# Kernel optimization log

Hardware: AMD Instinct MI355X
Metric: run time of the kernel (lower is better)

Reference implementation:

```python
import jax, jax.numpy as jnp
import numpy as np
import math

B, C, H, W = 512, 64, 8, 8
E, NH, MEM = 64, 8, 8          # embed_dim, num_heads, mem_n
HD = E // NH                   # head_dim
THD = H * W * HD               # tot_head_dim = 512
AMB = 5.0                      # attn_mask_b
LN_EPS = 1e-5


def conv2d(x, w, b):
    y = jax.lax.conv_general_dilated(x, w, (1, 1), 'SAME',
                                     dimension_numbers=('NCHW', 'OIHW', 'NCHW'))
    return y + b[None, :, None, None]


def setup_inputs() -> dict:
    key = jax.random.key(0)
    ks = jax.random.split(key, 14)
    r = lambda k, s, sc=1.0: jax.random.normal(k, s, dtype=jnp.float32) * sc
    return {
        'input': r(ks[0], (B, C, H, W)),
        'h_cur': r(ks[1], (B, E, H, W)),
        'c_cur': r(ks[2], (B, E, H, W)),
        'concat_k': r(ks[3], (B, MEM, NH, THD)),
        'concat_v': r(ks[4], (B, MEM, NH, THD)),
        'attn_mask': jax.random.randint(ks[5], (B * NH, 1, MEM), 0, 2).astype(bool),
        'conv_w': r(ks[6], (5 * E, C + E, 3, 3), 0.05),
        'conv_b': jnp.zeros((5 * E,), jnp.float32),
        'proj_w': r(ks[7], (3 * E, C, 3, 3), 0.05),
        'proj_b': jnp.zeros((3 * E,), jnp.float32),
        'out_w': r(ks[8], (E, E, 3, 3), 0.05),
        'out_b': jnp.zeros((E,), jnp.float32),
        'ln_w': jnp.ones((E, H, W), jnp.float32),
        'ln_b': jnp.zeros((E, H, W), jnp.float32),
        'pos_w': r(ks[9], (MEM, H * W * E), 0.02),
        'pos_b': jax.random.uniform(ks[10], (MEM, NH), jnp.float32, -0.1, 0.1),
    }


def _cell(input, h_cur, c_cur, concat_k, concat_v, attn_mask,
          conv_w, conv_b, proj_w, proj_b, out_w, out_b, ln_w, ln_b, pos_w, pos_b):
    # ConvLSTM gates
    combined = jnp.concatenate([input, h_cur], axis=1)          # [B, C+E, H, W]
    cc = conv2d(combined, conv_w, conv_b)                       # [B, 5E, H, W]
    cc_i, cc_f, cc_o, cc_g, cc_a = jnp.split(cc, 5, axis=1)
    i = jax.nn.sigmoid(cc_i)
    f = jax.nn.sigmoid(cc_f)
    o = jax.nn.sigmoid(cc_o)
    g = jnp.tanh(cc_g)
    a = jax.nn.sigmoid(cc_a)
    c_next = f * c_cur + i * g

    # attention over growing memory
    kqv = conv2d(input, proj_w, proj_b)                         # [B, 3E, H, W]
    k, q, v = jnp.split(kqv, 3, axis=1)
    # [B, E, H, W] -> [B*NH, 1, THD] (contiguous split of E into NH heads)
    resh = lambda x: x.reshape(B * NH, 1, THD)
    k, q, v = resh(k), resh(q), resh(v)
    q_scaled = q / math.sqrt(THD)

    # prior memory: [B, MEM, NH, THD] -> [B*NH, MEM-1, THD]
    def mem_resh(m):
        return jnp.transpose(m[:, 1:], (1, 0, 2, 3)).reshape(MEM - 1, B * NH, THD).transpose(1, 0, 2)
    k_full = jnp.concatenate([mem_resh(concat_k), k], axis=1)   # [B*NH, MEM, THD]
    v_full = jnp.concatenate([mem_resh(concat_v), v], axis=1)

    # learned positional key offsets / score biases
    pos_w_e = jnp.broadcast_to(pos_w[:, None, :], (MEM, B, H * W * E)) \
                 .reshape(MEM, B * NH, THD).transpose(1, 0, 2)  # [B*NH, MEM, THD]
    pos_b_e = jnp.broadcast_to(pos_b[:, None, :], (MEM, B, NH)) \
                 .reshape(MEM, B * NH).T                        # [B*NH, MEM]
    k_full = k_full + pos_w_e

    # additive mask: -inf where masked, last slot forced to +attn_mask_b
    mask = jnp.where(attn_mask, -jnp.inf, 0.0).astype(q.dtype)  # [B*NH, 1, MEM]
    mask = mask.at[:, :, -1].set(AMB)

    scores = mask + jnp.einsum('bqd,bkd->bqk', q_scaled, k_full) + pos_b_e[:, None, :]
    w = jax.nn.softmax(scores, axis=-1)                         # [B*NH, 1, MEM]
    attn = jnp.einsum('bqk,bkd->bqd', w, v_full)                # [B*NH, 1, THD]
    attn = attn.reshape(B, E, H, W)

    out = conv2d(attn, out_w, out_b) + input[:, :E]
    # LayerNorm over (E, H, W)
    mu = jnp.mean(out, axis=(1, 2, 3), keepdims=True)
    var = jnp.mean((out - mu) ** 2, axis=(1, 2, 3), keepdims=True)
    out = (out - mu) / jnp.sqrt(var + LN_EPS) * ln_w[None] + ln_b[None]

    c_next = c_next + a * jnp.tanh(out)
    h_next = o * jnp.tanh(c_next)

    ret = lambda m: m.transpose(1, 0, 2).reshape(MEM, B, NH, THD).transpose(1, 0, 2, 3)
    return h_next, c_next, ret(k_full), ret(v_full)


def reference(input, h_cur, c_cur, concat_k, concat_v, attn_mask,
              conv_w, conv_b, proj_w, proj_b, out_w, out_b, ln_w, ln_b, pos_w, pos_b):
    return _cell(input, h_cur, c_cur, concat_k, concat_v, attn_mask,
                 conv_w, conv_b, proj_w, proj_b, out_w, out_b, ln_w, ln_b, pos_w, pos_b)
```

## Files before the change

### kernel.cpp

```cpp
#include <hip/hip_runtime.h>

typedef short short8 __attribute__((ext_vector_type(8)));
typedef __bf16 bf16x8 __attribute__((ext_vector_type(8)));
typedef float f32x4 __attribute__((ext_vector_type(4)));

__device__ __forceinline__ short f2bf(float f) {
  unsigned u = __builtin_bit_cast(unsigned, f);
  u = (u + 0x7FFFu + ((u >> 16) & 1u)) >> 16;
  return (short)u;
}
__device__ __forceinline__ f32x4 mfma16(short8 a, short8 b, f32x4 c) {
  return __builtin_amdgcn_mfma_f32_16x16x32_bf16(
      __builtin_bit_cast(bf16x8, a), __builtin_bit_cast(bf16x8, b), c, 0, 0, 0);
}
__device__ __forceinline__ float sigm(float x) { return 1.0f / (1.0f + __expf(-x)); }
__device__ __forceinline__ float ftanh(float x) {
  return 1.0f - 2.0f / (1.0f + __expf(2.0f * x));
}
__device__ __forceinline__ f32x4 ntld4(const float* p) {
  return __builtin_nontemporal_load((const f32x4*)p);
}
__device__ __forceinline__ void ntst4(float* p, f32x4 v) {
  __builtin_nontemporal_store(v, (f32x4*)p);
}

__global__ void pack_w(const float* __restrict__ w1, const float* __restrict__ w2,
                       const float* __restrict__ w3, short* __restrict__ out) {
  int e = blockIdx.x * 256 + threadIdx.x;
  if (e < 46080) {
    int kb8 = e / 320, n = e % 320;
    short8 v;
#pragma unroll
    for (int j = 0; j < 8; ++j) {
      int k = kb8 * 8 + j;
      int tap = k >> 7, ci = k & 127;
      v[j] = f2bf(w1[(n * 128 + ci) * 9 + tap]);
    }
    *(short8*)&out[e * 8] = v;
    return;
  }
  e -= 46080;
  if (e < 13824) {
    int kb8 = e / 192, n = e % 192;
    short8 v;
#pragma unroll
    for (int j = 0; j < 8; ++j) {
      int k = kb8 * 8 + j;
      int tap = k >> 6, ci = k & 63;
      v[j] = f2bf(w2[(n * 64 + ci) * 9 + tap]);
    }
    *(short8*)&out[(46080 + e) * 8] = v;
    return;
  }
  e -= 13824;
  {
    int kb8 = e / 64, n = e % 64;
    short8 v;
#pragma unroll
    for (int j = 0; j < 8; ++j) {
      int k = kb8 * 8 + j;
      int tap = k >> 6, ci = k & 63;
      v[j] = f2bf(w3[(n * 64 + ci) * 9 + tap]);
    }
    *(short8*)&out[(46080 + 13824 + e) * 8] = v;
  }
}

__launch_bounds__(512, 4)
__global__ void kqv_k(const float* __restrict__ input,
                      const float* __restrict__ proj_b,
                      const float* __restrict__ pos_w,
                      const short* __restrict__ pk2,
                      float* __restrict__ q_out, float* __restrict__ o_k,
                      float* __restrict__ o_v) {
  __shared__ short comb[6400];
  __shared__ float Xk[4160], Xq[4160], Xv[4160];

  const int b = blockIdx.x;
  const int tid = threadIdx.x;
  const int wave = tid >> 6, lane = tid & 63;
  const int col = lane & 15, g4 = lane >> 4;
  const int wc = wave >> 1, wm = wave & 1;
  const int ch = wc * 16 + col;

#pragma unroll
  for (int i = 0; i < 2; ++i) {
    int idx = (tid + 512 * i) * 4;
    int c = idx >> 6, p0 = idx & 63;
    f32x4 vi = *(const f32x4*)&input[b * 4096 + idx];
#pragma unroll
    for (int j = 0; j < 4; ++j) {
      int p = p0 + j;
      int pp = ((p >> 3) + 1) * 10 + (p & 7) + 1;
      comb[pp * 64 + ((c + pp * 8) & 63)] = f2bf(vi[j]);
    }
  }
  for (int i = tid; i < 2304; i += 512) {
    int pr = i >> 6, c = i & 63;
    int pp = (pr < 10) ? pr
             : (pr < 20) ? (80 + pr)
             : (pr < 28) ? ((pr - 19) * 10)
                         : ((pr - 27) * 10 + 9);
    comb[pp * 64 + c] = 0;
  }
  __syncthreads();

  f32x4 acc2[2][3];
#pragma unroll
  for (int m = 0; m < 2; ++m)
#pragma unroll
    for (int g = 0; g < 3; ++g) acc2[m][g] = (f32x4){0.f, 0.f, 0.f, 0.f};

  short8 bb2[3];
#pragma unroll
  for (int g = 0; g < 3; ++g)
    bb2[g] = *(const short8*)&pk2[((g4)*192 + g * 64 + ch) * 8];

  for (int s = 0; s < 18; ++s) {
    short8 bbn[3];
    if (s < 17) {
      int kb8 = (s + 1) * 4 + g4;
#pragma unroll
      for (int g = 0; g < 3; ++g)
        bbn[g] = *(const short8*)&pk2[(kb8 * 192 + g * 64 + ch) * 8];
    }
    int tap = s >> 1, cib = s & 1;
    int kh = tap / 3, kw = tap % 3;
    short8 a[2];
#pragma unroll
    for (int m = 0; m < 2; ++m) {
      int p = (wm * 2 + m) * 16 + col;
      int pp = ((p >> 3) + kh) * 10 + (p & 7) + kw;
      int slot = (cib * 32 + g4 * 8 + pp * 8) & 63;
      a[m] = *(const short8*)&comb[pp * 64 + slot];
    }
#pragma unroll
    for (int m = 0; m < 2; ++m)
#pragma unroll
      for (int g = 0; g < 3; ++g) acc2[m][g] = mfma16(a[m], bb2[g], acc2[m][g]);
    if (s < 17) {
#pragma unroll
      for (int g = 0; g < 3; ++g) bb2[g] = bbn[g];
    }
  }
  {
    float pb0 = proj_b[ch], pb1 = proj_b[64 + ch], pb2 = proj_b[128 + ch];
    const float rsq = 0.044194173824159216f;
#pragma unroll
    for (int m = 0; m < 2; ++m)
#pragma unroll
      for (int r = 0; r < 4; ++r) {
        int p = (wm * 2 + m) * 16 + g4 * 4 + r;
        Xk[ch * 65 + p] = acc2[m][0][r] + pb0 + pos_w[7 * 4096 + ch * 64 + p];
        Xq[ch * 65 + p] = (acc2[m][1][r] + pb1) * rsq;
        Xv[ch * 65 + p] = acc2[m][2][r] + pb2;
      }
  }
  __syncthreads();

  const size_t base7 = (size_t)(b * 64 + 56) * 512;
#pragma unroll
  for (int i = 0; i < 2; ++i) {
    int idx = (tid + 512 * i) * 4;
    int c = idx >> 6, p0 = idx & 63;
    f32x4 kq, qq, vq;
#pragma unroll
    for (int j = 0; j < 4; ++j) {
      kq[j] = Xk[c * 65 + p0 + j];
      qq[j] = Xq[c * 65 + p0 + j];
      vq[j] = Xv[c * 65 + p0 + j];
    }
    *(f32x4*)&o_k[base7 + idx] = kq;
    *(f32x4*)&q_out[(size_t)b * 4096 + idx] = qq;
    *(f32x4*)&o_v[base7 + idx] = vq;
  }
}

__launch_bounds__(64, 4)
__global__ void attn_k(const float* __restrict__ ck, const float* __restrict__ cv,
                       const int* __restrict__ amask,
                       const float* __restrict__ pos_w,
                       const float* __restrict__ pos_b,
                       const float* __restrict__ q_in,
                       float* __restrict__ o_k, float* __restrict__ o_v,
                       float* __restrict__ attn_out) {
  const int b = blockIdx.x >> 3;
  const int hd = blockIdx.x & 7;
  const int lane = threadIdx.x;
  const int d0 = lane * 4, d1 = (lane + 64) * 4;

  const float* qp = q_in + (size_t)b * 4096 + hd * 512;
  f32x4 q0 = *(const f32x4*)&qp[d0];
  f32x4 q1 = *(const f32x4*)&qp[d1];

  float sc[8];
#pragma unroll
  for (int m = 0; m < 7; ++m) {
    const float* kp = ck + ((size_t)((b * 8 + m + 1) * 8 + hd)) * 512;
    const float* pw = pos_w + m * 4096 + hd * 512;
    f32x4 k0 = ntld4(kp + d0) + *(const f32x4*)&pw[d0];
    f32x4 k1 = ntld4(kp + d1) + *(const f32x4*)&pw[d1];
    float* dst = o_k + ((size_t)((b * 8 + m) * 8 + hd)) * 512;
    ntst4(dst + d0, k0);
    ntst4(dst + d1, k1);
    float part = 0.f;
#pragma unroll
    for (int j = 0; j < 4; ++j) {
      part = fmaf(q0[j], k0[j], part);
      part = fmaf(q1[j], k1[j], part);
    }
#pragma unroll
    for (int off = 32; off >= 1; off >>= 1) part += __shfl_xor(part, off);
    float msk = amask[(b * 8 + hd) * 8 + m] ? -__builtin_inff() : 0.0f;
    sc[m] = part + pos_b[m * 8 + hd] + msk;
  }
  {
    const float* kp = o_k + ((size_t)((b * 8 + 7) * 8 + hd)) * 512;
    f32x4 k0 = *(const f32x4*)&kp[d0];
    f32x4 k1 = *(const f32x4*)&kp[d1];
    float part = 0.f;
#pragma unroll
    for (int j = 0; j < 4; ++j) {
      part = fmaf(q0[j], k0[j], part);
      part = fmaf(q1[j], k1[j], part);
    }
#pragma unroll
    for (int off = 32; off >= 1; off >>= 1) part += __shfl_xor(part, off);
    sc[7] = part + pos_b[7 * 8 + hd] + 5.0f;
  }

  float mx = sc[0];
#pragma unroll
  for (int m = 1; m < 8; ++m) mx = fmaxf(mx, sc[m]);
  float w[8], s = 0.f;
#pragma unroll
  for (int m = 0; m < 8; ++m) {
    w[m] = __expf(sc[m] - mx);
    s += w[m];
  }
  float inv = 1.0f / s;
#pragma unroll
  for (int m = 0; m < 8; ++m) w[m] *= inv;

  f32x4 a0 = (f32x4){0.f, 0.f, 0.f, 0.f};
  f32x4 a1 = (f32x4){0.f, 0.f, 0.f, 0.f};
#pragma unroll
  for (int m = 0; m < 7; ++m) {
    const float* vp = cv + ((size_t)((b * 8 + m + 1) * 8 + hd)) * 512;
    f32x4 v0 = ntld4(vp + d0);
    f32x4 v1 = ntld4(vp + d1);
    float* dst = o_v + ((size_t)((b * 8 + m) * 8 + hd)) * 512;
    ntst4(dst + d0, v0);
    ntst4(dst + d1, v1);
    a0 += v0 * w[m];
    a1 += v1 * w[m];
  }
  {
    const float* vp = o_v + ((size_t)((b * 8 + 7) * 8 + hd)) * 512;
    a0 += *(const f32x4*)&vp[d0] * w[7];
    a1 += *(const f32x4*)&vp[d1] * w[7];
  }
  float* ap = attn_out + (size_t)b * 4096 + hd * 512;
  *(f32x4*)&ap[d0] = a0;
  *(f32x4*)&ap[d1] = a1;
}

__launch_bounds__(512, 4)
__global__ void cell2_k(
    const float* __restrict__ input, const float* __restrict__ h_cur,
    const float* __restrict__ c_cur, const float* __restrict__ attn_in,
    const float* __restrict__ conv_b, const float* __restrict__ out_b,
    const float* __restrict__ ln_w, const float* __restrict__ ln_b,
    const short* __restrict__ pk1, const short* __restrict__ pk3,
    float* __restrict__ o_h, float* __restrict__ o_c) {
  __shared__ short comb[12800];
  __shared__ float Xb[4160];
  __shared__ float Qb[4160];
  __shared__ float Vb[4160];
  __shared__ float red[16];

  const int b = blockIdx.x;
  const int tid = threadIdx.x;
  const int wave = tid >> 6, lane = tid & 63;
  const int col = lane & 15, g4 = lane >> 4;
  const int wc = wave >> 1, wm = wave & 1;
  const int ch = wc * 16 + col;

#pragma unroll
  for (int i = 0; i < 2; ++i) {
    int idx = (tid + 512 * i) * 4;
    int c = idx >> 6, p0 = idx & 63;
    f32x4 vi = *(const f32x4*)&input[b * 4096 + idx];
    f32x4 vh = *(const f32x4*)&h_cur[b * 4096 + idx];
    f32x4 vc = *(const f32x4*)&c_cur[b * 4096 + idx];
#pragma unroll
    for (int j = 0; j < 4; ++j) {
      int p = p0 + j;
      int pp = ((p >> 3) + 1) * 10 + (p & 7) + 1;
      comb[pp * 128 + ((c + pp * 8) & 127)] = f2bf(vi[j]);
      comb[pp * 128 + ((c + 64 + pp * 8) & 127)] = f2bf(vh[j]);
      Xb[c * 65 + p] = vc[j];
    }
  }
  for (int i = tid; i < 4608; i += 512) {
    int pr = i >> 7, c = i & 127;
    int pp = (pr < 10) ? pr
             : (pr < 20) ? (80 + pr)
             : (pr < 28) ? ((pr - 19) * 10)
                         : ((pr - 27) * 10 + 9);
    comb[pp * 128 + c] = 0;
  }
  __syncthreads();

  f32x4 acc1[2][5];
#pragma unroll
  for (int m = 0; m < 2; ++m)
#pragma unroll
    for (int g = 0; g < 5; ++g) acc1[m][g] = (f32x4){0.f, 0.f, 0.f, 0.f};

  short8 bb1[5];
#pragma unroll
  for (int g = 0; g < 5; ++g)
    bb1[g] = *(const short8*)&pk1[((g4)*320 + g * 64 + ch) * 8];

  for (int s = 0; s < 36; ++s) {
    short8 bbn[5];
    if (s < 35) {
      int kb8 = (s + 1) * 4 + g4;
#pragma unroll
      for (int g = 0; g < 5; ++g)
        bbn[g] = *(const short8*)&pk1[(kb8 * 320 + g * 64 + ch) * 8];
    }
    int tap = s >> 2, cib = s & 3;
    int kh = tap / 3, kw = tap % 3;
    short8 a[2];
#pragma unroll
    for (int m = 0; m < 2; ++m) {
      int p = (wm * 2 + m) * 16 + col;
      int pp = ((p >> 3) + kh) * 10 + (p & 7) + kw;
      int slot = (cib * 32 + g4 * 8 + pp * 8) & 127;
      a[m] = *(const short8*)&comb[pp * 128 + slot];
    }
#pragma unroll
    for (int m = 0; m < 2; ++m)
#pragma unroll
      for (int g = 0; g < 5; ++g) acc1[m][g] = mfma16(a[m], bb1[g], acc1[m][g]);
    if (s < 35) {
#pragma unroll
      for (int g = 0; g < 5; ++g) bb1[g] = bbn[g];
    }
  }

  float ct_r[8], o_r[8], a_r[8];
  {
    float bi0 = conv_b[ch], bi1 = conv_b[64 + ch], bi2 = conv_b[128 + ch];
    float bi3 = conv_b[192 + ch], bi4 = conv_b[256 + ch];
#pragma unroll
    for (int m = 0; m < 2; ++m)
#pragma unroll
      for (int r = 0; r < 4; ++r) {
        int p = (wm * 2 + m) * 16 + g4 * 4 + r;
        float iv = sigm(acc1[m][0][r] + bi0);
        float fv = sigm(acc1[m][1][r] + bi1);
        float ov = sigm(acc1[m][2][r] + bi2);
        float gv = ftanh(acc1[m][3][r] + bi3);
        float av = sigm(acc1[m][4][r] + bi4);
        ct_r[m * 4 + r] = fv * Xb[ch * 65 + p] + iv * gv;
        o_r[m * 4 + r] = ov;
        a_r[m * 4 + r] = av;
      }
  }
  __syncthreads();

  {
    f32x4 av[2], iv[2];
#pragma unroll
    for (int i = 0; i < 2; ++i) {
      int idx = (tid + 512 * i) * 4;
      av[i] = *(const f32x4*)&attn_in[b * 4096 + idx];
      iv[i] = *(const f32x4*)&input[b * 4096 + idx];
    }
#pragma unroll
    for (int i = 0; i < 2; ++i) {
      int idx = (tid + 512 * i) * 4;
      int c = idx >> 6, p0 = idx & 63;
#pragma unroll
      for (int j = 0; j < 4; ++j) {
        int p = p0 + j;
        int pp = ((p >> 3) + 1) * 10 + (p & 7) + 1;
        comb[pp * 128 + ((c + pp * 8) & 127)] = f2bf(av[i][j]);
        Xb[c * 65 + p] = iv[i][j];
      }
    }
  }
  __syncthreads();

  f32x4 acc3[2];
  acc3[0] = (f32x4){0.f, 0.f, 0.f, 0.f};
  acc3[1] = (f32x4){0.f, 0.f, 0.f, 0.f};
  short8 bb3 = *(const short8*)&pk3[((g4)*64 + ch) * 8];
  for (int s = 0; s < 18; ++s) {
    short8 bbn;
    if (s < 17) {
      int kb8 = (s + 1) * 4 + g4;
      bbn = *(const short8*)&pk3[(kb8 * 64 + ch) * 8];
    }
    int tap = s >> 1, cib = s & 1;
    int kh = tap / 3, kw = tap % 3;
    short8 a[2];
#pragma unroll
    for (int m = 0; m < 2; ++m) {
      int p = (wm * 2 + m) * 16 + col;
      int pp = ((p >> 3) + kh) * 10 + (p & 7) + kw;
      int slot = (cib * 32 + g4 * 8 + pp * 8) & 127;
      a[m] = *(const short8*)&comb[pp * 128 + slot];
    }
#pragma unroll
    for (int m = 0; m < 2; ++m) acc3[m] = mfma16(a[m], bb3, acc3[m]);
    if (s < 17) bb3 = bbn;
  }

  float ov_[8], s1 = 0.f, s2 = 0.f;
  {
    float ob = out_b[ch];
#pragma unroll
    for (int m = 0; m < 2; ++m)
#pragma unroll
      for (int r = 0; r < 4; ++r) {
        int p = (wm * 2 + m) * 16 + g4 * 4 + r;
        float v = acc3[m][r] + ob + Xb[ch * 65 + p];
        ov_[m * 4 + r] = v;
        s1 += v;
        s2 += v * v;
      }
  }
#pragma unroll
  for (int off = 32; off >= 1; off >>= 1) {
    s1 += __shfl_xor(s1, off);
    s2 += __shfl_xor(s2, off);
  }
  if (lane == 0) { red[wave] = s1; red[8 + wave] = s2; }
  __syncthreads();
  float ts1 = 0.f, ts2 = 0.f;
#pragma unroll
  for (int w = 0; w < 8; ++w) { ts1 += red[w]; ts2 += red[8 + w]; }
  float mu = ts1 * (1.0f / 4096.0f);
  float var = ts2 * (1.0f / 4096.0f) - mu * mu;
  float rstd = rsqrtf(var + 1e-5f);

#pragma unroll
  for (int m = 0; m < 2; ++m)
#pragma unroll
    for (int r = 0; r < 4; ++r) {
      int p = (wm * 2 + m) * 16 + g4 * 4 + r;
      float oln = (ov_[m * 4 + r] - mu) * rstd * ln_w[ch * 64 + p] + ln_b[ch * 64 + p];
      float cn = ct_r[m * 4 + r] + a_r[m * 4 + r] * ftanh(oln);
      float hv = o_r[m * 4 + r] * ftanh(cn);
      Qb[ch * 65 + p] = hv;
      Vb[ch * 65 + p] = cn;
    }
  __syncthreads();
#pragma unroll
  for (int i = 0; i < 2; ++i) {
    int idx = (tid + 512 * i) * 4;
    int c = idx >> 6, p0 = idx & 63;
    f32x4 hv, cvv;
#pragma unroll
    for (int j = 0; j < 4; ++j) {
      hv[j] = Qb[c * 65 + p0 + j];
      cvv[j] = Vb[c * 65 + p0 + j];
    }
    *(f32x4*)&o_h[b * 4096 + idx] = hv;
    *(f32x4*)&o_c[b * 4096 + idx] = cvv;
  }
}

extern "C" void kernel_launch(void* const* d_in, const int* in_sizes, int n_in,
                              void* d_out, int out_size, void* d_ws, size_t ws_size,
                              hipStream_t stream) {
  (void)in_sizes; (void)n_in; (void)out_size; (void)ws_size;
  const float* input  = (const float*)d_in[0];
  const float* h_cur  = (const float*)d_in[1];
  const float* c_cur  = (const float*)d_in[2];
  const float* ck     = (const float*)d_in[3];
  const float* cv     = (const float*)d_in[4];
  const int*   amask  = (const int*)d_in[5];
  const float* conv_w = (const float*)d_in[6];
  const float* conv_b = (const float*)d_in[7];
  const float* proj_w = (const float*)d_in[8];
  const float* proj_b = (const float*)d_in[9];
  const float* out_w  = (const float*)d_in[10];
  const float* out_b  = (const float*)d_in[11];
  const float* ln_w   = (const float*)d_in[12];
  const float* ln_b   = (const float*)d_in[13];
  const float* pos_w  = (const float*)d_in[14];
  const float* pos_b  = (const float*)d_in[15];

  short* pk = (short*)d_ws;
  float* o_h = (float*)d_out;
  float* o_c = o_h + 2097152;
  float* o_k = o_h + 4194304;
  float* o_v = o_h + 20971520;

  pack_w<<<252, 256, 0, stream>>>(conv_w, proj_w, out_w, pk);
  kqv_k<<<512, 512, 0, stream>>>(input, proj_b, pos_w, pk + 368640,
                                 o_h, o_k, o_v);
  attn_k<<<4096, 64, 0, stream>>>(ck, cv, amask, pos_w, pos_b, o_h,
                                  o_k, o_v, o_c);
  cell2_k<<<512, 512, 0, stream>>>(input, h_cur, c_cur, o_c,
                                   conv_b, out_b, ln_w, ln_b,
                                   pk, pk + 479232, o_h, o_c);
}
```

Before: 113.7 us.

## Restructure into mid kernel fusing kqv+attention alongside gate conv, plus back kernel

Replaces the kqv/attn/cell2 chain with two kernels. The first runs 1024 blocks: half compute the k/q/v projection conv and then the full attention per batch item in the same block, and the other half compute the ConvLSTM gate conv, writing c_t and packed bf16 o/a gates to workspace. The second kernel does the output conv, LayerNorm and the final cell update. This removes one launch and the q round-trip through global memory, and lets the gate conv run concurrently with attention. In exchange it adds workspace traffic for the attention output, c_t and gates, stores gates and attention output in bf16 (lower precision), and falls back to the old path when the workspace is too small.

```diff
diff --git a/kernel.cpp b/kernel.cpp
--- a/kernel.cpp
+++ b/kernel.cpp
@@ -3,6 +3,8 @@
 typedef short short8 __attribute__((ext_vector_type(8)));
 typedef __bf16 bf16x8 __attribute__((ext_vector_type(8)));
 typedef float f32x4 __attribute__((ext_vector_type(4)));
+typedef short s16x4 __attribute__((ext_vector_type(4)));
+typedef unsigned u32x4 __attribute__((ext_vector_type(4)));
 
 __device__ __forceinline__ short f2bf(float f) {
   unsigned u = __builtin_bit_cast(unsigned, f);
@@ -63,6 +65,490 @@
       v[j] = f2bf(w3[(n * 64 + ci) * 9 + tap]);
     }
     *(short8*)&out[(46080 + 13824 + e) * 8] = v;
+  }
+}
+
+
+__launch_bounds__(512, 4)
+__global__ void mid_k(const float* __restrict__ input, const float* __restrict__ h_cur,
+                      const float* __restrict__ c_cur, const float* __restrict__ ck,
+                      const float* __restrict__ cv, const int* __restrict__ amask,
+                      const float* __restrict__ conv_b, const float* __restrict__ proj_b,
+                      const float* __restrict__ pos_w, const float* __restrict__ pos_b,
+                      const short* __restrict__ pk1, const short* __restrict__ pk2,
+                      float* __restrict__ o_k, float* __restrict__ o_v,
+                      short* __restrict__ ws_attn, float* __restrict__ ws_ct,
+                      unsigned* __restrict__ ws_oa) {
+  __shared__ short comb[12800];
+  __shared__ float Xb[4160];
+  __shared__ float sc_lds[8];
+  float* combf = (float*)comb;
+  unsigned* Xbu = (unsigned*)Xb;
+
+  const int tid = threadIdx.x;
+  const int wave = tid >> 6, lane = tid & 63;
+  const int col = lane & 15, g4 = lane >> 4;
+  const int wc = wave >> 1, wm = wave & 1;
+  const int ch = wc * 16 + col;
+
+  if (blockIdx.x < 512) {
+    const int b = blockIdx.x;
+    if (tid < 8) sc_lds[tid] = 0.f;
+
+#pragma unroll
+    for (int i = 0; i < 2; ++i) {
+      int idx = (tid + 512 * i) * 4;
+      int c = idx >> 6, p0 = idx & 63;
+      f32x4 vi = *(const f32x4*)&input[b * 4096 + idx];
+#pragma unroll
+      for (int j = 0; j < 4; ++j) {
+        int p = p0 + j;
+        int pp = ((p >> 3) + 1) * 10 + (p & 7) + 1;
+        comb[pp * 64 + ((c + pp * 8) & 63)] = f2bf(vi[j]);
+      }
+    }
+    for (int i = tid; i < 2304; i += 512) {
+      int pr = i >> 6, c = i & 63;
+      int pp = (pr < 10) ? pr
+               : (pr < 20) ? (80 + pr)
+               : (pr < 28) ? ((pr - 19) * 10)
+                           : ((pr - 27) * 10 + 9);
+      comb[pp * 64 + c] = 0;
+    }
+    __syncthreads();
+
+    f32x4 acc2[2][3];
+#pragma unroll
+    for (int m = 0; m < 2; ++m)
+#pragma unroll
+      for (int g = 0; g < 3; ++g) acc2[m][g] = (f32x4){0.f, 0.f, 0.f, 0.f};
+    short8 bb2[3];
+#pragma unroll
+    for (int g = 0; g < 3; ++g)
+      bb2[g] = *(const short8*)&pk2[((g4)*192 + g * 64 + ch) * 8];
+    for (int s = 0; s < 18; ++s) {
+      short8 bbn[3];
+      if (s < 17) {
+        int kb8 = (s + 1) * 4 + g4;
+#pragma unroll
+        for (int g = 0; g < 3; ++g)
+          bbn[g] = *(const short8*)&pk2[(kb8 * 192 + g * 64 + ch) * 8];
+      }
+      int tap = s >> 1, cib = s & 1;
+      int kh = tap / 3, kw = tap % 3;
+      short8 a[2];
+#pragma unroll
+      for (int m = 0; m < 2; ++m) {
+        int p = (wm * 2 + m) * 16 + col;
+        int pp = ((p >> 3) + kh) * 10 + (p & 7) + kw;
+        int slot = (cib * 32 + g4 * 8 + pp * 8) & 63;
+        a[m] = *(const short8*)&comb[pp * 64 + slot];
+      }
+#pragma unroll
+      for (int m = 0; m < 2; ++m)
+#pragma unroll
+        for (int g = 0; g < 3; ++g) acc2[m][g] = mfma16(a[m], bb2[g], acc2[m][g]);
+      if (s < 17) {
+#pragma unroll
+        for (int g = 0; g < 3; ++g) bb2[g] = bbn[g];
+      }
+    }
+
+    float kreg[8], qreg[8], vreg[8], part7 = 0.f;
+    {
+      float pb0 = proj_b[ch], pb1 = proj_b[64 + ch], pb2 = proj_b[128 + ch];
+      const float rsq = 0.044194173824159216f;
+#pragma unroll
+      for (int m = 0; m < 2; ++m)
+#pragma unroll
+        for (int r = 0; r < 4; ++r) {
+          int p = (wm * 2 + m) * 16 + g4 * 4 + r;
+          float kf = acc2[m][0][r] + pb0 + pos_w[7 * 4096 + ch * 64 + p];
+          float qf = (acc2[m][1][r] + pb1) * rsq;
+          float vf = acc2[m][2][r] + pb2;
+          kreg[m * 4 + r] = kf;
+          qreg[m * 4 + r] = qf;
+          vreg[m * 4 + r] = vf;
+          part7 = fmaf(qf, kf, part7);
+        }
+    }
+    atomicAdd(&sc_lds[ch >> 3], part7);
+    __syncthreads();
+
+#pragma unroll
+    for (int m = 0; m < 2; ++m)
+#pragma unroll
+      for (int r = 0; r < 4; ++r) {
+        int p = (wm * 2 + m) * 16 + g4 * 4 + r;
+        combf[ch * 65 + p] = kreg[m * 4 + r];
+        Xb[ch * 65 + p] = qreg[m * 4 + r];
+      }
+    __syncthreads();
+
+    const size_t base7 = (size_t)(b * 64 + 56) * 512;
+#pragma unroll
+    for (int i = 0; i < 2; ++i) {
+      int idx = (tid + 512 * i) * 4;
+      int c = idx >> 6, p0 = idx & 63;
+      f32x4 kq;
+#pragma unroll
+      for (int j = 0; j < 4; ++j) kq[j] = combf[c * 65 + p0 + j];
+      ntst4(&o_k[base7 + idx], kq);
+    }
+    const int hd = wave;
+    const int d0 = lane * 4, d1 = (lane + 64) * 4;
+    const int cs0 = d0 >> 6, po0 = d0 & 63, cs1 = d1 >> 6, po1 = d1 & 63;
+    f32x4 q0, q1;
+#pragma unroll
+    for (int j = 0; j < 4; ++j) {
+      q0[j] = Xb[(hd * 8 + cs0) * 65 + po0 + j];
+      q1[j] = Xb[(hd * 8 + cs1) * 65 + po1 + j];
+    }
+    float sc7 = sc_lds[hd] + pos_b[7 * 8 + hd] + 5.0f;
+    __syncthreads();
+
+#pragma unroll
+    for (int m = 0; m < 2; ++m)
+#pragma unroll
+      for (int r = 0; r < 4; ++r) {
+        int p = (wm * 2 + m) * 16 + g4 * 4 + r;
+        combf[ch * 65 + p] = vreg[m * 4 + r];
+      }
+    __syncthreads();
+#pragma unroll
+    for (int i = 0; i < 2; ++i) {
+      int idx = (tid + 512 * i) * 4;
+      int c = idx >> 6, p0 = idx & 63;
+      f32x4 vq;
+#pragma unroll
+      for (int j = 0; j < 4; ++j) vq[j] = combf[c * 65 + p0 + j];
+      ntst4(&o_v[base7 + idx], vq);
+    }
+    f32x4 v70, v71;
+#pragma unroll
+    for (int j = 0; j < 4; ++j) {
+      v70[j] = combf[(hd * 8 + cs0) * 65 + po0 + j];
+      v71[j] = combf[(hd * 8 + cs1) * 65 + po1 + j];
+    }
+
+    float scv[8];
+    scv[7] = sc7;
+#pragma unroll
+    for (int m = 0; m < 7; ++m) {
+      const float* kp = ck + ((size_t)((b * 8 + m + 1) * 8 + hd)) * 512;
+      const float* pw = pos_w + m * 4096 + hd * 512;
+      f32x4 k0 = ntld4(kp + d0) + *(const f32x4*)&pw[d0];
+      f32x4 k1 = ntld4(kp + d1) + *(const f32x4*)&pw[d1];
+      float* dst = o_k + ((size_t)((b * 8 + m) * 8 + hd)) * 512;
+      ntst4(dst + d0, k0);
+      ntst4(dst + d1, k1);
+      float part = 0.f;
+#pragma unroll
+      for (int j = 0; j < 4; ++j) {
+        part = fmaf(q0[j], k0[j], part);
+        part = fmaf(q1[j], k1[j], part);
+      }
+#pragma unroll
+      for (int off = 32; off >= 1; off >>= 1) part += __shfl_xor(part, off);
+      float msk = amask[(b * 8 + hd) * 8 + m] ? -__builtin_inff() : 0.0f;
+      scv[m] = part + pos_b[m * 8 + hd] + msk;
+    }
+    float mx = scv[0];
+#pragma unroll
+    for (int m = 1; m < 8; ++m) mx = fmaxf(mx, scv[m]);
+    float w[8], s = 0.f;
+#pragma unroll
+    for (int m = 0; m < 8; ++m) {
+      w[m] = __expf(scv[m] - mx);
+      s += w[m];
+    }
+    float inv = 1.0f / s;
+#pragma unroll
+    for (int m = 0; m < 8; ++m) w[m] *= inv;
+
+    f32x4 a0 = (f32x4){0.f, 0.f, 0.f, 0.f};
+    f32x4 a1 = (f32x4){0.f, 0.f, 0.f, 0.f};
+#pragma unroll
+    for (int m = 0; m < 7; ++m) {
+      const float* vp = cv + ((size_t)((b * 8 + m + 1) * 8 + hd)) * 512;
+      f32x4 v0 = ntld4(vp + d0);
+      f32x4 v1 = ntld4(vp + d1);
+      float* dst = o_v + ((size_t)((b * 8 + m) * 8 + hd)) * 512;
+      ntst4(dst + d0, v0);
+      ntst4(dst + d1, v1);
+      a0 += v0 * w[m];
+      a1 += v1 * w[m];
+    }
+    a0 += v70 * w[7];
+    a1 += v71 * w[7];
+
+    s16x4 s0, s1;
+#pragma unroll
+    for (int j = 0; j < 4; ++j) {
+      s0[j] = f2bf(a0[j]);
+      s1[j] = f2bf(a1[j]);
+    }
+    *(s16x4*)&ws_attn[(size_t)b * 4096 + hd * 512 + d0] = s0;
+    *(s16x4*)&ws_attn[(size_t)b * 4096 + hd * 512 + d1] = s1;
+  } else {
+    const int b = blockIdx.x - 512;
+#pragma unroll
+    for (int i = 0; i < 2; ++i) {
+      int idx = (tid + 512 * i) * 4;
+      int c = idx >> 6, p0 = idx & 63;
+      f32x4 vi = *(const f32x4*)&input[b * 4096 + idx];
+      f32x4 vh = *(const f32x4*)&h_cur[b * 4096 + idx];
+      f32x4 vc = *(const f32x4*)&c_cur[b * 4096 + idx];
+#pragma unroll
+      for (int j = 0; j < 4; ++j) {
+        int p = p0 + j;
+        int pp = ((p >> 3) + 1) * 10 + (p & 7) + 1;
+        comb[pp * 128 + ((c + pp * 8) & 127)] = f2bf(vi[j]);
+        comb[pp * 128 + ((c + 64 + pp * 8) & 127)] = f2bf(vh[j]);
+        Xb[c * 65 + p] = vc[j];
+      }
+    }
+    for (int i = tid; i < 4608; i += 512) {
+      int pr = i >> 7, c = i & 127;
+      int pp = (pr < 10) ? pr
+               : (pr < 20) ? (80 + pr)
+               : (pr < 28) ? ((pr - 19) * 10)
+                           : ((pr - 27) * 10 + 9);
+      comb[pp * 128 + c] = 0;
+    }
+    __syncthreads();
+
+    f32x4 acc1[2][5];
+#pragma unroll
+    for (int m = 0; m < 2; ++m)
+#pragma unroll
+      for (int g = 0; g < 5; ++g) acc1[m][g] = (f32x4){0.f, 0.f, 0.f, 0.f};
+    short8 bb1[5];
+#pragma unroll
+    for (int g = 0; g < 5; ++g)
+      bb1[g] = *(const short8*)&pk1[((g4)*320 + g * 64 + ch) * 8];
+    for (int s = 0; s < 36; ++s) {
+      short8 bbn[5];
+      if (s < 35) {
+        int kb8 = (s + 1) * 4 + g4;
+#pragma unroll
+        for (int g = 0; g < 5; ++g)
+          bbn[g] = *(const short8*)&pk1[(kb8 * 320 + g * 64 + ch) * 8];
+      }
+      int tap = s >> 2, cib = s & 3;
+      int kh = tap / 3, kw = tap % 3;
+      short8 a[2];
+#pragma unroll
+      for (int m = 0; m < 2; ++m) {
+        int p = (wm * 2 + m) * 16 + col;
+        int pp = ((p >> 3) + kh) * 10 + (p & 7) + kw;
+        int slot = (cib * 32 + g4 * 8 + pp * 8) & 127;
+        a[m] = *(const short8*)&comb[pp * 128 + slot];
+      }
+#pragma unroll
+      for (int m = 0; m < 2; ++m)
+#pragma unroll
+        for (int g = 0; g < 5; ++g) acc1[m][g] = mfma16(a[m], bb1[g], acc1[m][g]);
+      if (s < 35) {
+#pragma unroll
+        for (int g = 0; g < 5; ++g) bb1[g] = bbn[g];
+      }
+    }
+
+    float ctv[8];
+    unsigned oav[8];
+    {
+      float bi0 = conv_b[ch], bi1 = conv_b[64 + ch], bi2 = conv_b[128 + ch];
+      float bi3 = conv_b[192 + ch], bi4 = conv_b[256 + ch];
+#pragma unroll
+      for (int m = 0; m < 2; ++m)
+#pragma unroll
+        for (int r = 0; r < 4; ++r) {
+          int p = (wm * 2 + m) * 16 + g4 * 4 + r;
+          float iv = sigm(acc1[m][0][r] + bi0);
+          float fv = sigm(acc1[m][1][r] + bi1);
+          float ov = sigm(acc1[m][2][r] + bi2);
+          float gv = ftanh(acc1[m][3][r] + bi3);
+          float av = sigm(acc1[m][4][r] + bi4);
+          ctv[m * 4 + r] = fv * Xb[ch * 65 + p] + iv * gv;
+          oav[m * 4 + r] = ((unsigned)(unsigned short)f2bf(av) << 16) |
+                           (unsigned)(unsigned short)f2bf(ov);
+        }
+    }
+    __syncthreads();
+#pragma unroll
+    for (int m = 0; m < 2; ++m)
+#pragma unroll
+      for (int r = 0; r < 4; ++r) {
+        int p = (wm * 2 + m) * 16 + g4 * 4 + r;
+        combf[ch * 65 + p] = ctv[m * 4 + r];
+        Xbu[ch * 65 + p] = oav[m * 4 + r];
+      }
+    __syncthreads();
+#pragma unroll
+    for (int i = 0; i < 2; ++i) {
+      int idx = (tid + 512 * i) * 4;
+      int c = idx >> 6, p0 = idx & 63;
+      f32x4 cq;
+      u32x4 oq;
+#pragma unroll
+      for (int j = 0; j < 4; ++j) {
+        cq[j] = combf[c * 65 + p0 + j];
+        oq[j] = Xbu[c * 65 + p0 + j];
+      }
+      *(f32x4*)&ws_ct[(size_t)b * 4096 + idx] = cq;
+      *(u32x4*)&ws_oa[(size_t)b * 4096 + idx] = oq;
+    }
+  }
+}
+
+__launch_bounds__(512, 4)
+__global__ void back_k(const float* __restrict__ input,
+                       const short* __restrict__ ws_attn,
+                       const float* __restrict__ ws_ct,
+                       const unsigned* __restrict__ ws_oa,
+                       const float* __restrict__ out_b,
+                       const float* __restrict__ ln_w, const float* __restrict__ ln_b,
+                       const short* __restrict__ pk3,
+                       float* __restrict__ o_h, float* __restrict__ o_c) {
+  __shared__ short comb[8320];
+  __shared__ float Xb[4160];
+  __shared__ float red[16];
+  float* combf = (float*)comb;
+  unsigned* Xbu = (unsigned*)Xb;
+
+  const int b = blockIdx.x;
+  const int tid = threadIdx.x;
+  const int wave = tid >> 6, lane = tid & 63;
+  const int col = lane & 15, g4 = lane >> 4;
+  const int wc = wave >> 1, wm = wave & 1;
+  const int ch = wc * 16 + col;
+
+  f32x4 ctr[2];
+  u32x4 oar[2];
+#pragma unroll
+  for (int i = 0; i < 2; ++i) {
+    int idx = (tid + 512 * i) * 4;
+    ctr[i] = *(const f32x4*)&ws_ct[(size_t)b * 4096 + idx];
+    oar[i] = *(const u32x4*)&ws_oa[(size_t)b * 4096 + idx];
+  }
+#pragma unroll
+  for (int i = 0; i < 2; ++i) {
+    int idx = (tid + 512 * i) * 4;
+    int c = idx >> 6, p0 = idx & 63;
+    s16x4 av = *(const s16x4*)&ws_attn[(size_t)b * 4096 + idx];
+    f32x4 vi = *(const f32x4*)&input[b * 4096 + idx];
+#pragma unroll
+    for (int j = 0; j < 4; ++j) {
+      int p = p0 + j;
+      int pp = ((p >> 3) + 1) * 10 + (p & 7) + 1;
+      comb[pp * 64 + ((c + pp * 8) & 63)] = av[j];
+      Xb[c * 65 + p] = vi[j];
+    }
+  }
+  for (int i = tid; i < 2304; i += 512) {
+    int pr = i >> 6, c = i & 63;
+    int pp = (pr < 10) ? pr
+             : (pr < 20) ? (80 + pr)
+             : (pr < 28) ? ((pr - 19) * 10)
+                         : ((pr - 27) * 10 + 9);
+    comb[pp * 64 + c] = 0;
+  }
+  __syncthreads();
+
+  f32x4 acc3[2];
+  acc3[0] = (f32x4){0.f, 0.f, 0.f, 0.f};
+  acc3[1] = (f32x4){0.f, 0.f, 0.f, 0.f};
+  short8 bb3 = *(const short8*)&pk3[((g4)*64 + ch) * 8];
+  for (int s = 0; s < 18; ++s) {
+    short8 bbn;
+    if (s < 17) {
+      int kb8 = (s + 1) * 4 + g4;
+      bbn = *(const short8*)&pk3[(kb8 * 64 + ch) * 8];
+    }
+    int tap = s >> 1, cib = s & 1;
+    int kh = tap / 3, kw = tap % 3;
+    short8 a[2];
+#pragma unroll
+    for (int m = 0; m < 2; ++m) {
+      int p = (wm * 2 + m) * 16 + col;
+      int pp = ((p >> 3) + kh) * 10 + (p & 7) + kw;
+      int slot = (cib * 32 + g4 * 8 + pp * 8) & 63;
+      a[m] = *(const short8*)&comb[pp * 64 + slot];
+    }
+#pragma unroll
+    for (int m = 0; m < 2; ++m) acc3[m] = mfma16(a[m], bb3, acc3[m]);
+    if (s < 17) bb3 = bbn;
+  }
+
+  float ov_[8], s1 = 0.f, s2 = 0.f;
+  {
+    float ob = out_b[ch];
+#pragma unroll
+    for (int m = 0; m < 2; ++m)
+#pragma unroll
+      for (int r = 0; r < 4; ++r) {
+        int p = (wm * 2 + m) * 16 + g4 * 4 + r;
+        float v = acc3[m][r] + ob + Xb[ch * 65 + p];
+        ov_[m * 4 + r] = v;
+        s1 += v;
+        s2 += v * v;
+      }
+  }
+#pragma unroll
+  for (int off = 32; off >= 1; off >>= 1) {
+    s1 += __shfl_xor(s1, off);
+    s2 += __shfl_xor(s2, off);
+  }
+  if (lane == 0) { red[wave] = s1; red[8 + wave] = s2; }
+  __syncthreads();
+  float ts1 = 0.f, ts2 = 0.f;
+#pragma unroll
+  for (int w = 0; w < 8; ++w) { ts1 += red[w]; ts2 += red[8 + w]; }
+  float mu = ts1 * (1.0f / 4096.0f);
+  float var = ts2 * (1.0f / 4096.0f) - mu * mu;
+  float rstd = rsqrtf(var + 1e-5f);
+
+#pragma unroll
+  for (int i = 0; i < 2; ++i) {
+    int idx = (tid + 512 * i) * 4;
+    int c = idx >> 6, p0 = idx & 63;
+#pragma unroll
+    for (int j = 0; j < 4; ++j) {
+      combf[c * 65 + p0 + j] = ctr[i][j];
+      Xbu[c * 65 + p0 + j] = oar[i][j];
+    }
+  }
+  __syncthreads();
+
+#pragma unroll
+  for (int m = 0; m < 2; ++m)
+#pragma unroll
+    for (int r = 0; r < 4; ++r) {
+      int p = (wm * 2 + m) * 16 + g4 * 4 + r;
+      float ct = combf[ch * 65 + p];
+      unsigned u = Xbu[ch * 65 + p];
+      float og = __builtin_bit_cast(float, u << 16);
+      float ag = __builtin_bit_cast(float, u & 0xffff0000u);
+      float oln = (ov_[m * 4 + r] - mu) * rstd * ln_w[ch * 64 + p] + ln_b[ch * 64 + p];
+      float cn = ct + ag * ftanh(oln);
+      float hv = og * ftanh(cn);
+      combf[ch * 65 + p] = hv;
+      Xb[ch * 65 + p] = cn;
+    }
+  __syncthreads();
+#pragma unroll
+  for (int i = 0; i < 2; ++i) {
+    int idx = (tid + 512 * i) * 4;
+    int c = idx >> 6, p0 = idx & 63;
+    f32x4 hq, cq;
+#pragma unroll
+    for (int j = 0; j < 4; ++j) {
+      hq[j] = combf[c * 65 + p0 + j];
+      cq[j] = Xb[c * 65 + p0 + j];
+    }
+    *(f32x4*)&o_h[b * 4096 + idx] = hq;
+    *(f32x4*)&o_c[b * 4096 + idx] = cq;
   }
 }
 
@@ -75,14 +561,12 @@
                       float* __restrict__ o_v) {
   __shared__ short comb[6400];
   __shared__ float Xk[4160], Xq[4160], Xv[4160];
-
   const int b = blockIdx.x;
   const int tid = threadIdx.x;
   const int wave = tid >> 6, lane = tid & 63;
   const int col = lane & 15, g4 = lane >> 4;
   const int wc = wave >> 1, wm = wave & 1;
   const int ch = wc * 16 + col;
-
 #pragma unroll
   for (int i = 0; i < 2; ++i) {
     int idx = (tid + 512 * i) * 4;
@@ -104,18 +588,15 @@
     comb[pp * 64 + c] = 0;
   }
   __syncthreads();
-
   f32x4 acc2[2][3];
 #pragma unroll
   for (int m = 0; m < 2; ++m)
 #pragma unroll
     for (int g = 0; g < 3; ++g) acc2[m][g] = (f32x4){0.f, 0.f, 0.f, 0.f};
-
   short8 bb2[3];
 #pragma unroll
   for (int g = 0; g < 3; ++g)
     bb2[g] = *(const short8*)&pk2[((g4)*192 + g * 64 + ch) * 8];
-
   for (int s = 0; s < 18; ++s) {
     short8 bbn[3];
     if (s < 17) {
@@ -157,7 +638,6 @@
       }
   }
   __syncthreads();
-
   const size_t base7 = (size_t)(b * 64 + 56) * 512;
 #pragma unroll
   for (int i = 0; i < 2; ++i) {
@@ -188,11 +668,9 @@
   const int hd = blockIdx.x & 7;
   const int lane = threadIdx.x;
   const int d0 = lane * 4, d1 = (lane + 64) * 4;
-
   const float* qp = q_in + (size_t)b * 4096 + hd * 512;
   f32x4 q0 = *(const f32x4*)&qp[d0];
   f32x4 q1 = *(const f32x4*)&qp[d1];
-
   float sc[8];
 #pragma unroll
   for (int m = 0; m < 7; ++m) {
@@ -228,7 +706,6 @@
     for (int off = 32; off >= 1; off >>= 1) part += __shfl_xor(part, off);
     sc[7] = part + pos_b[7 * 8 + hd] + 5.0f;
   }
-
   float mx = sc[0];
 #pragma unroll
   for (int m = 1; m < 8; ++m) mx = fmaxf(mx, sc[m]);
@@ -241,7 +718,6 @@
   float inv = 1.0f / s;
 #pragma unroll
   for (int m = 0; m < 8; ++m) w[m] *= inv;
-
   f32x4 a0 = (f32x4){0.f, 0.f, 0.f, 0.f};
   f32x4 a1 = (f32x4){0.f, 0.f, 0.f, 0.f};
 #pragma unroll
@@ -278,14 +754,12 @@
   __shared__ float Qb[4160];
   __shared__ float Vb[4160];
   __shared__ float red[16];
-
   const int b = blockIdx.x;
   const int tid = threadIdx.x;
   const int wave = tid >> 6, lane = tid & 63;
   const int col = lane & 15, g4 = lane >> 4;
   const int wc = wave >> 1, wm = wave & 1;
   const int ch = wc * 16 + col;
-
 #pragma unroll
   for (int i = 0; i < 2; ++i) {
     int idx = (tid + 512 * i) * 4;
@@ -311,18 +785,15 @@
     comb[pp * 128 + c] = 0;
   }
   __syncthreads();
-
   f32x4 acc1[2][5];
 #pragma unroll
   for (int m = 0; m < 2; ++m)
 #pragma unroll
     for (int g = 0; g < 5; ++g) acc1[m][g] = (f32x4){0.f, 0.f, 0.f, 0.f};
-
   short8 bb1[5];
 #pragma unroll
   for (int g = 0; g < 5; ++g)
     bb1[g] = *(const short8*)&pk1[((g4)*320 + g * 64 + ch) * 8];
-
   for (int s = 0; s < 36; ++s) {
     short8 bbn[5];
     if (s < 35) {
@@ -350,7 +821,6 @@
       for (int g = 0; g < 5; ++g) bb1[g] = bbn[g];
     }
   }
-
   float ct_r[8], o_r[8], a_r[8];
   {
     float bi0 = conv_b[ch], bi1 = conv_b[64 + ch], bi2 = conv_b[128 + ch];
@@ -371,7 +841,6 @@
       }
   }
   __syncthreads();
-
   {
     f32x4 av[2], iv[2];
 #pragma unroll
@@ -394,7 +863,6 @@
     }
   }
   __syncthreads();
-
   f32x4 acc3[2];
   acc3[0] = (f32x4){0.f, 0.f, 0.f, 0.f};
   acc3[1] = (f32x4){0.f, 0.f, 0.f, 0.f};
@@ -419,7 +887,6 @@
     for (int m = 0; m < 2; ++m) acc3[m] = mfma16(a[m], bb3, acc3[m]);
     if (s < 17) bb3 = bbn;
   }
-
   float ov_[8], s1 = 0.f, s2 = 0.f;
   {
     float ob = out_b[ch];
@@ -447,7 +914,6 @@
   float mu = ts1 * (1.0f / 4096.0f);
   float var = ts2 * (1.0f / 4096.0f) - mu * mu;
   float rstd = rsqrtf(var + 1e-5f);
-
 #pragma unroll
   for (int m = 0; m < 2; ++m)
 #pragma unroll
@@ -478,7 +944,7 @@
 extern "C" void kernel_launch(void* const* d_in, const int* in_sizes, int n_in,
                               void* d_out, int out_size, void* d_ws, size_t ws_size,
                               hipStream_t stream) {
-  (void)in_sizes; (void)n_in; (void)out_size; (void)ws_size;
+  (void)in_sizes; (void)n_in; (void)out_size;
   const float* input  = (const float*)d_in[0];
   const float* h_cur  = (const float*)d_in[1];
   const float* c_cur  = (const float*)d_in[2];
@@ -496,18 +962,32 @@
   const float* pos_w  = (const float*)d_in[14];
   const float* pos_b  = (const float*)d_in[15];
 
-  short* pk = (short*)d_ws;
+  char* ws = (char*)d_ws;
+  short* pk = (short*)ws;
   float* o_h = (float*)d_out;
   float* o_c = o_h + 2097152;
   float* o_k = o_h + 4194304;
   float* o_v = o_h + 20971520;
 
   pack_w<<<252, 256, 0, stream>>>(conv_w, proj_w, out_w, pk);
-  kqv_k<<<512, 512, 0, stream>>>(input, proj_b, pos_w, pk + 368640,
-                                 o_h, o_k, o_v);
-  attn_k<<<4096, 64, 0, stream>>>(ck, cv, amask, pos_w, pos_b, o_h,
-                                  o_k, o_v, o_c);
-  cell2_k<<<512, 512, 0, stream>>>(input, h_cur, c_cur, o_c,
-                                   conv_b, out_b, ln_w, ln_b,
-                                   pk, pk + 479232, o_h, o_c);
-}
+
+  if (ws_size >= (24u << 20)) {
+    short* ws_attn = (short*)(ws + (2u << 20));
+    float* ws_ct = (float*)(ws + (8u << 20));
+    unsigned* ws_oa = (unsigned*)(ws + (16u << 20));
+    mid_k<<<1024, 512, 0, stream>>>(input, h_cur, c_cur, ck, cv, amask,
+                                    conv_b, proj_b, pos_w, pos_b,
+                                    pk, pk + 368640,
+                                    o_k, o_v, ws_attn, ws_ct, ws_oa);
+    back_k<<<512, 512, 0, stream>>>(input, ws_attn, ws_ct, ws_oa,
+                                    out_b, ln_w, ln_b, pk + 479232, o_h, o_c);
+  } else {
+    kqv_k<<<512, 512, 0, stream>>>(input, proj_b, pos_w, pk + 368640,
+                                   o_h, o_k, o_v);
+    attn_k<<<4096, 64, 0, stream>>>(ck, cv, amask, pos_w, pos_b, o_h,
+                                    o_k, o_v, o_c);
+    cell2_k<<<512, 512, 0, stream>>>(input, h_cur, c_cur, o_c,
+                                     conv_b, out_b, ln_w, ln_b,
+                                     pk, pk + 479232, o_h, o_c);
+  }
+}
```

After: 109.2 us. 1.04x faster.
